# Optimization experiments

Measured on AMD Instinct MI355X. Metric: run time of the kernel, lower is better.

## Reference

```python
import jax, jax.numpy as jnp
import numpy as np

EPSILON_BASE = 0.1
N_ITERS = 10


def setup_inputs() -> dict:
    key = jax.random.key(0)
    k1, k2 = jax.random.split(key)
    N, D = 8192, 512
    embeddings = jax.random.normal(k1, (N, D), dtype=jnp.float32)
    target_noise = jax.random.normal(k2, (N, D), dtype=jnp.float32)
    return {"embeddings": embeddings, "target_noise": target_noise}


def _l2_normalize(x, axis=1, eps=1e-12):
    # matches torch.nn.functional.normalize (divide by max(norm, eps))
    norm = jnp.sqrt(jnp.sum(x * x, axis=axis, keepdims=True))
    return x / jnp.maximum(norm, eps)


def _sinkhorn(x, y):
    n, d = x.shape
    # normalize_embeddings=True path
    x = _l2_normalize(x, axis=1)
    y = _l2_normalize(y, axis=1)
    epsilon = EPSILON_BASE * 2.0
    # squared euclidean cost: C[i,j] = ||x_i - y_j||^2  (cdist p=2, squared)
    sq_x = jnp.sum(x * x, axis=1, keepdims=True)          # (n,1)
    sq_y = jnp.sum(y * y, axis=1, keepdims=True)          # (n,1)
    C = jnp.maximum(sq_x + sq_y.T - 2.0 * (x @ y.T), 0.0)  # (n,n)
    log_K = -C / epsilon

    def body(carry, _):
        log_u, log_v = carry
        log_u = -jax.nn.logsumexp(log_K + log_v[None, :], axis=1)
        log_v = -jax.nn.logsumexp(log_K.T + log_u[None, :], axis=1)
        return (log_u, log_v), None

    init = (jnp.zeros(n, dtype=x.dtype), jnp.zeros(n, dtype=y.dtype))
    (log_u, log_v), _ = jax.lax.scan(body, init, None, length=N_ITERS)

    log_P = log_u[:, None] + log_K + log_v[None, :]
    P = jnp.clip(jnp.exp(log_P), 0.0, 1.0)
    distance = jnp.sum(P * C) / n

    # nan/inf fallback: 1 - mean cosine similarity (x, y already unit norm)
    fallback = 1.0 - jnp.mean(jnp.sum(x * y, axis=1))
    bad = jnp.isnan(distance) | jnp.isinf(distance)
    return jnp.where(bad, fallback, distance)


def reference(embeddings, target_noise):
    if embeddings.ndim == 3:
        embeddings = embeddings.reshape(-1, embeddings.shape[-1])
        target_noise = target_noise.reshape(-1, target_noise.shape[-1])
    return _sinkhorn(embeddings, target_noise)
```

## Files before the change

kernel.cpp:

```cpp
#include <hip/hip_runtime.h>
#include <hip/hip_bf16.h>
#include <stdint.h>

#define NROW 8192
#define DIM  512
#define LN2   0.6931471805599453f
#define TEN_LOG2E 14.426950408889634f

typedef __attribute__((ext_vector_type(8))) short short8;
typedef __attribute__((ext_vector_type(4))) float f32x4;
typedef __attribute__((ext_vector_type(2))) float f32x2;

__global__ __launch_bounds__(256) void init_kernel(float* __restrict__ v,
                                                   float* __restrict__ diagacc,
                                                   float* __restrict__ distacc) {
  const int g = blockIdx.x * 256 + threadIdx.x;
  v[g] = 1.0f;
  if (g == 0) { diagacc[0] = 0.f; distacc[0] = 0.f; }
}

__global__ __launch_bounds__(256) void normalize_kernel(
    const float* __restrict__ X, const float* __restrict__ Y,
    __hip_bfloat16* __restrict__ Xn, __hip_bfloat16* __restrict__ Yn,
    float* __restrict__ diagacc) {
  const int wave = threadIdx.x >> 6, lane = threadIdx.x & 63;
  float dsum = 0.f;
  #pragma unroll
  for (int rr = 0; rr < 4; rr++) {
    const int row = blockIdx.x * 16 + wave * 4 + rr;
    const float4* xr = (const float4*)(X + (size_t)row * DIM);
    const float4* yr = (const float4*)(Y + (size_t)row * DIM);
    float4 x0 = xr[lane], x1 = xr[lane + 64];
    float4 y0 = yr[lane], y1 = yr[lane + 64];
    float sx = x0.x*x0.x + x0.y*x0.y + x0.z*x0.z + x0.w*x0.w
             + x1.x*x1.x + x1.y*x1.y + x1.z*x1.z + x1.w*x1.w;
    float sy = y0.x*y0.x + y0.y*y0.y + y0.z*y0.z + y0.w*y0.w
             + y1.x*y1.x + y1.y*y1.y + y1.z*y1.z + y1.w*y1.w;
    float sxy = x0.x*y0.x + x0.y*y0.y + x0.z*y0.z + x0.w*y0.w
              + x1.x*y1.x + x1.y*y1.y + x1.z*y1.z + x1.w*y1.w;
    #pragma unroll
    for (int off = 1; off < 64; off <<= 1) {
      sx  += __shfl_xor(sx, off, 64);
      sy  += __shfl_xor(sy, off, 64);
      sxy += __shfl_xor(sxy, off, 64);
    }
    const float rx = 1.0f / fmaxf(sqrtf(sx), 1e-12f);
    const float ry = 1.0f / fmaxf(sqrtf(sy), 1e-12f);
    if (lane == 0) dsum += sxy * rx * ry;
    ushort4 px, py;
    { __hip_bfloat16 b;
      b = __float2bfloat16(x0.x*rx); px.x = *(unsigned short*)&b;
      b = __float2bfloat16(x0.y*rx); px.y = *(unsigned short*)&b;
      b = __float2bfloat16(x0.z*rx); px.z = *(unsigned short*)&b;
      b = __float2bfloat16(x0.w*rx); px.w = *(unsigned short*)&b;
      b = __float2bfloat16(y0.x*ry); py.x = *(unsigned short*)&b;
      b = __float2bfloat16(y0.y*ry); py.y = *(unsigned short*)&b;
      b = __float2bfloat16(y0.z*ry); py.z = *(unsigned short*)&b;
      b = __float2bfloat16(y0.w*ry); py.w = *(unsigned short*)&b;
    }
    ((ushort4*)(Xn + (size_t)row * DIM))[lane] = px;
    ((ushort4*)(Yn + (size_t)row * DIM))[lane] = py;
    { __hip_bfloat16 b;
      b = __float2bfloat16(x1.x*rx); px.x = *(unsigned short*)&b;
      b = __float2bfloat16(x1.y*rx); px.y = *(unsigned short*)&b;
      b = __float2bfloat16(x1.z*rx); px.z = *(unsigned short*)&b;
      b = __float2bfloat16(x1.w*rx); px.w = *(unsigned short*)&b;
      b = __float2bfloat16(y1.x*ry); py.x = *(unsigned short*)&b;
      b = __float2bfloat16(y1.y*ry); py.y = *(unsigned short*)&b;
      b = __float2bfloat16(y1.z*ry); py.z = *(unsigned short*)&b;
      b = __float2bfloat16(y1.w*ry); py.w = *(unsigned short*)&b;
    }
    ((ushort4*)(Xn + (size_t)row * DIM))[lane + 64] = px;
    ((ushort4*)(Yn + (size_t)row * DIM))[lane + 64] = py;
  }
  if (lane == 0) atomicAdd(diagacc, dsum);
}

__global__ __launch_bounds__(256) void gemm_kernel(
    const __hip_bfloat16* __restrict__ A, const __hip_bfloat16* __restrict__ B,
    uint8_t* __restrict__ K) {
  __shared__ __align__(16) char smem[20480];
  short* As = (short*)smem;
  short* Bs = (short*)(smem + 10240);
  int* tileT = (int*)smem;

  const int m0 = blockIdx.y * 128;
  const int n0 = blockIdx.x * 128;
  const int t = threadIdx.x;
  const int wave = t >> 6, lane = t & 63;
  const int wm = (wave & 1) * 64, wn = (wave >> 1) * 64;
  const int fr = lane & 15;
  const int fq = lane >> 4;

  f32x4 acc[4][4];
  #pragma unroll
  for (int i = 0; i < 4; i++)
    #pragma unroll
    for (int j = 0; j < 4; j++) acc[i][j] = (f32x4)0.f;

  const int L0 = t, L1 = t + 256;
  const int ar0 = L0 >> 2, ac0 = L0 & 3;
  const int ar1 = L1 >> 2, ac1 = L1 & 3;
  const int4* Ag = (const int4*)A;
  const int4* Bg = (const int4*)B;

  for (int kt = 0; kt < 16; ++kt) {
    const int kb = kt * 4;
    int4 a0 = Ag[(size_t)(m0 + ar0) * 64 + kb + ac0];
    int4 a1 = Ag[(size_t)(m0 + ar1) * 64 + kb + ac1];
    int4 b0 = Bg[(size_t)(n0 + ar0) * 64 + kb + ac0];
    int4 b1 = Bg[(size_t)(n0 + ar1) * 64 + kb + ac1];
    __syncthreads();
    ((int4*)As)[ar0 * 5 + ac0] = a0;
    ((int4*)As)[ar1 * 5 + ac1] = a1;
    ((int4*)Bs)[ar0 * 5 + ac0] = b0;
    ((int4*)Bs)[ar1 * 5 + ac1] = b1;
    __syncthreads();
    short8 af[4], bfr[4];
    #pragma unroll
    for (int i = 0; i < 4; i++) {
      af[i]  = *(const short8*)&As[(wm + i * 16 + fr) * 40 + fq * 8];
      bfr[i] = *(const short8*)&Bs[(wn + i * 16 + fr) * 40 + fq * 8];
    }
    #pragma unroll
    for (int i = 0; i < 4; i++)
      #pragma unroll
      for (int j = 0; j < 4; j++)
        acc[i][j] = __builtin_amdgcn_mfma_f32_16x16x32_bf16(af[i], bfr[j], acc[i][j], 0, 0, 0);
  }
  __syncthreads();
  #pragma unroll
  for (int i = 0; i < 4; i++) {
    #pragma unroll
    for (int j = 0; j < 4; j++) {
      const int Rq = (wm >> 2) + i * 4 + fq;
      const int Cc = wn + j * 16 + fr;
      float v0 = exp2f(fminf(acc[i][j][0], 1.0f) * TEN_LOG2E);
      float v1 = exp2f(fminf(acc[i][j][1], 1.0f) * TEN_LOG2E);
      float v2 = exp2f(fminf(acc[i][j][2], 1.0f) * TEN_LOG2E);
      float v3 = exp2f(fminf(acc[i][j][3], 1.0f) * TEN_LOG2E);
      int pk = 0;
      pk = __builtin_amdgcn_cvt_pk_fp8_f32(v0, v1, pk, false);
      pk = __builtin_amdgcn_cvt_pk_fp8_f32(v2, v3, pk, true);
      tileT[Cc * 33 + Rq] = pk;
    }
  }
  __syncthreads();
  const int rl = t >> 1;
  const int half = t & 1;
  const int rq = rl >> 2;
  const int rb = (rl & 3) * 8;
  uint8_t* Krow = K + (size_t)(m0 + rl) * NROW + n0 + half * 64;
  #pragma unroll
  for (int q = 0; q < 4; q++) {
    int out[4];
    #pragma unroll
    for (int d = 0; d < 4; d++) {
      const int c0 = (half * 16 + q * 4 + d) * 4;
      const unsigned w0 = (unsigned)tileT[(c0 + 0) * 33 + rq];
      const unsigned w1 = (unsigned)tileT[(c0 + 1) * 33 + rq];
      const unsigned w2 = (unsigned)tileT[(c0 + 2) * 33 + rq];
      const unsigned w3 = (unsigned)tileT[(c0 + 3) * 33 + rq];
      out[d] = (int)(((w0 >> rb) & 0xffu) | (((w1 >> rb) & 0xffu) << 8)
                   | (((w2 >> rb) & 0xffu) << 16) | (((w3 >> rb) & 0xffu) << 24));
    }
    int4 o; o.x = out[0]; o.y = out[1]; o.z = out[2]; o.w = out[3];
    ((int4*)Krow)[q] = o;
  }
}

__global__ __launch_bounds__(512) void fused_pass_kernel(
    const uint8_t* __restrict__ K, const float* __restrict__ v,
    float* __restrict__ u, float* __restrict__ partials) {
  __shared__ float wsum[8][8];
  __shared__ float ubc[8];
  const int t = threadIdx.x;
  const int wave = t >> 6, lane = t & 63;
  const int i0 = blockIdx.x * 32;

  float wv[16];
  {
    const float4* vp = (const float4*)(v + t * 16);
    ((float4*)wv)[0] = vp[0]; ((float4*)wv)[1] = vp[1];
    ((float4*)wv)[2] = vp[2]; ((float4*)wv)[3] = vp[3];
  }
  float acc[16];
  #pragma unroll
  for (int c = 0; c < 16; c++) acc[c] = 0.f;

  for (int b = 0; b < 4; b++) {
    const int rbase = i0 + b * 8;
    int4 kd[8];
    #pragma unroll
    for (int r = 0; r < 8; r++)
      kd[r] = *(const int4*)(K + (size_t)(rbase + r) * NROW + t * 16);
    float dot[8];
    #pragma unroll
    for (int r = 0; r < 8; r++) {
      const int* kp = (const int*)&kd[r];
      float d0 = 0.f, d1 = 0.f;
      #pragma unroll
      for (int q = 0; q < 4; q++) {
        f32x2 lo = __builtin_amdgcn_cvt_pk_f32_fp8(kp[q], false);
        f32x2 hi = __builtin_amdgcn_cvt_pk_f32_fp8(kp[q], true);
        d0 += lo.x * wv[4 * q] + lo.y * wv[4 * q + 1];
        d1 += hi.x * wv[4 * q + 2] + hi.y * wv[4 * q + 3];
      }
      dot[r] = d0 + d1;
    }
    #pragma unroll
    for (int r = 0; r < 8; r++)
      #pragma unroll
      for (int off = 1; off < 64; off <<= 1)
        dot[r] += __shfl_xor(dot[r], off, 64);
    if (lane == 0) {
      #pragma unroll
      for (int r = 0; r < 8; r++) wsum[wave][r] = dot[r];
    }
    __syncthreads();
    if (t < 8) {
      float s = wsum[0][t] + wsum[1][t] + wsum[2][t] + wsum[3][t]
              + wsum[4][t] + wsum[5][t] + wsum[6][t] + wsum[7][t];
      float uu = 1.0f / s;
      ubc[t] = uu;
      u[rbase + t] = uu;
    }
    __syncthreads();
    float ur[8];
    #pragma unroll
    for (int r = 0; r < 8; r++) ur[r] = ubc[r];
    #pragma unroll
    for (int r = 0; r < 8; r++) {
      const int* kp = (const int*)&kd[r];
      #pragma unroll
      for (int q = 0; q < 4; q++) {
        f32x2 lo = __builtin_amdgcn_cvt_pk_f32_fp8(kp[q], false);
        f32x2 hi = __builtin_amdgcn_cvt_pk_f32_fp8(kp[q], true);
        acc[4 * q]     += lo.x * ur[r];
        acc[4 * q + 1] += lo.y * ur[r];
        acc[4 * q + 2] += hi.x * ur[r];
        acc[4 * q + 3] += hi.y * ur[r];
      }
    }
  }
  float4* pp = (float4*)(partials + (size_t)blockIdx.x * NROW + t * 16);
  pp[0] = ((float4*)acc)[0]; pp[1] = ((float4*)acc)[1];
  pp[2] = ((float4*)acc)[2]; pp[3] = ((float4*)acc)[3];
}

__global__ __launch_bounds__(256) void vreduce_kernel(
    const float* __restrict__ partials, float* __restrict__ v) {
  const int j = blockIdx.x * 256 + threadIdx.x;
  float s = 0.f;
  #pragma unroll 8
  for (int p = 0; p < 256; p++) s += partials[(size_t)p * NROW + j];
  v[j] = 1.0f / s;
}

__global__ __launch_bounds__(512) void dist_kernel(
    const uint8_t* __restrict__ K, const float* __restrict__ v,
    const float* __restrict__ u, float* __restrict__ distacc) {
  __shared__ float uld[32];
  const int t = threadIdx.x;
  const int i0 = blockIdx.x * 32;
  if (t < 32) uld[t] = u[i0 + t];
  float wv[16];
  {
    const float4* vp = (const float4*)(v + t * 16);
    ((float4*)wv)[0] = vp[0]; ((float4*)wv)[1] = vp[1];
    ((float4*)wv)[2] = vp[2]; ((float4*)wv)[3] = vp[3];
  }
  __syncthreads();
  float acc = 0.f;
  #pragma unroll 4
  for (int r = 0; r < 32; r++) {
    int4 kd = *(const int4*)(K + (size_t)(i0 + r) * NROW + t * 16);
    const float ui = uld[r];
    const int* kp = (const int*)&kd;
    #pragma unroll
    for (int q = 0; q < 4; q++) {
      f32x2 lo = __builtin_amdgcn_cvt_pk_f32_fp8(kp[q], false);
      f32x2 hi = __builtin_amdgcn_cvt_pk_f32_fp8(kp[q], true);
      float kvv[4] = {lo.x, lo.y, hi.x, hi.y};
      #pragma unroll
      for (int e = 0; e < 4; e++) {
        float kk = kvv[e];
        float p = fminf(ui * kk * wv[4 * q + e], 1.f);
        float ct = 2.f - 0.2f * LN2 * __log2f(fmaxf(kk, 1e-6f));
        acc += p * ct;
      }
    }
  }
  #pragma unroll
  for (int off = 32; off > 0; off >>= 1) acc += __shfl_down(acc, off, 64);
  __shared__ float sb[8];
  const int wave = t >> 6;
  if ((t & 63) == 0) sb[wave] = acc;
  __syncthreads();
  if (t == 0) {
    float tot = sb[0] + sb[1] + sb[2] + sb[3] + sb[4] + sb[5] + sb[6] + sb[7];
    atomicAdd(distacc, tot);
  }
}

__global__ void final_kernel(const float* __restrict__ distacc,
                             const float* __restrict__ diagacc,
                             float* __restrict__ out) {
  if (threadIdx.x == 0 && blockIdx.x == 0) {
    float d = distacc[0] * (1.0f / (float)NROW);
    float fb = 1.0f - diagacc[0] * (1.0f / (float)NROW);
    float v = (isnan(d) || isinf(d)) ? fb : d;
    __hip_bfloat16 b = __float2bfloat16(v);
    unsigned short h = *(unsigned short*)&b;
    ((unsigned int*)out)[0] = ((unsigned int)h << 16) | (unsigned int)h;
  }
}

extern "C" void kernel_launch(void* const* d_in, const int* in_sizes, int n_in,
                              void* d_out, int out_size, void* d_ws, size_t ws_size,
                              hipStream_t stream) {
  (void)in_sizes; (void)n_in; (void)out_size; (void)ws_size;
  const float* X = (const float*)d_in[0];
  const float* Y = (const float*)d_in[1];
  float* out = (float*)d_out;

  char* ws = (char*)d_ws;
  size_t off = 0;
  uint8_t* K = (uint8_t*)(ws + off);                off += (size_t)NROW * NROW;
  float* partials = (float*)(ws + off);             off += (size_t)256 * NROW * 4;
  __hip_bfloat16* Xn = (__hip_bfloat16*)(ws + off); off += (size_t)NROW * DIM * 2;
  __hip_bfloat16* Yn = (__hip_bfloat16*)(ws + off); off += (size_t)NROW * DIM * 2;
  float* uvec = (float*)(ws + off); off += NROW * 4;
  float* vvec = (float*)(ws + off); off += NROW * 4;
  float* diagacc = (float*)(ws + off); off += 256;
  float* distacc = (float*)(ws + off); off += 256;

  init_kernel<<<32, 256, 0, stream>>>(vvec, diagacc, distacc);
  normalize_kernel<<<512, 256, 0, stream>>>(X, Y, Xn, Yn, diagacc);
  gemm_kernel<<<dim3(64, 64), 256, 0, stream>>>(Xn, Yn, K);
  for (int it = 0; it < 10; ++it) {
    fused_pass_kernel<<<256, 512, 0, stream>>>(K, vvec, uvec, partials);
    vreduce_kernel<<<32, 256, 0, stream>>>(partials, vvec);
  }
  dist_kernel<<<256, 512, 0, stream>>>(K, vvec, uvec, distacc);
  final_kernel<<<1, 64, 0, stream>>>(distacc, diagacc, out);
}
```

Before: 539.1 us.

## Async LDS loads in GEMM, wider blocks and prefetch in Sinkhorn passes

The GEMM now stages A/B tiles through global_load_lds direct-to-LDS copies with a 64-wide K step, and the epilogue transpose uses a row-major tile read back with vector loads. The fused Sinkhorn pass moves to 1024-thread blocks with 8 bytes per thread and double-buffers the K row loads for the next 8-row group. The vreduce kernel splits each column's 256-partial sum across 8 thread groups in 256 blocks, and dist_kernel is widened the same way. The aim is more memory-level parallelism and lower latency, at the cost of unpadded LDS layouts that may cause bank conflicts and higher register pressure.

```diff
diff --git a/kernel.cpp b/kernel.cpp
--- a/kernel.cpp
+++ b/kernel.cpp
@@ -10,6 +10,16 @@
 typedef __attribute__((ext_vector_type(8))) short short8;
 typedef __attribute__((ext_vector_type(4))) float f32x4;
 typedef __attribute__((ext_vector_type(2))) float f32x2;
+
+__device__ __forceinline__ void barrier_lgkm() {
+  asm volatile("s_waitcnt lgkmcnt(0)\n\ts_barrier" ::: "memory");
+}
+
+__device__ __forceinline__ void async_copy16(void* lds, const void* g) {
+  __builtin_amdgcn_global_load_lds((const __attribute__((address_space(1))) void*)g,
+                                   (__attribute__((address_space(3))) void*)lds,
+                                   16, 0, 0);
+}
 
 __global__ __launch_bounds__(256) void init_kernel(float* __restrict__ v,
                                                    float* __restrict__ diagacc,
@@ -79,9 +89,9 @@
 __global__ __launch_bounds__(256) void gemm_kernel(
     const __hip_bfloat16* __restrict__ A, const __hip_bfloat16* __restrict__ B,
     uint8_t* __restrict__ K) {
-  __shared__ __align__(16) char smem[20480];
-  short* As = (short*)smem;
-  short* Bs = (short*)(smem + 10240);
+  __shared__ __align__(16) char smem[32768];
+  short* As_s = (short*)smem;
+  short* Bs_s = (short*)(smem + 16384);
   int* tileT = (int*)smem;
 
   const int m0 = blockIdx.y * 128;
@@ -98,35 +108,38 @@
     #pragma unroll
     for (int j = 0; j < 4; j++) acc[i][j] = (f32x4)0.f;
 
-  const int L0 = t, L1 = t + 256;
-  const int ar0 = L0 >> 2, ac0 = L0 & 3;
-  const int ar1 = L1 >> 2, ac1 = L1 & 3;
-  const int4* Ag = (const int4*)A;
-  const int4* Bg = (const int4*)B;
-
-  for (int kt = 0; kt < 16; ++kt) {
-    const int kb = kt * 4;
-    int4 a0 = Ag[(size_t)(m0 + ar0) * 64 + kb + ac0];
-    int4 a1 = Ag[(size_t)(m0 + ar1) * 64 + kb + ac1];
-    int4 b0 = Bg[(size_t)(n0 + ar0) * 64 + kb + ac0];
-    int4 b1 = Bg[(size_t)(n0 + ar1) * 64 + kb + ac1];
+  const char* Ab = (const char*)A;
+  const char* Bb = (const char*)B;
+  const int trow = t >> 3;
+  const int tcol = (t & 7) * 16;
+  char* AsB = (char*)As_s;
+  char* BsB = (char*)Bs_s;
+
+  for (int kt = 0; kt < 8; ++kt) {
     __syncthreads();
-    ((int4*)As)[ar0 * 5 + ac0] = a0;
-    ((int4*)As)[ar1 * 5 + ac1] = a1;
-    ((int4*)Bs)[ar0 * 5 + ac0] = b0;
-    ((int4*)Bs)[ar1 * 5 + ac1] = b1;
+    const size_t koff = (size_t)kt * 128 + tcol;
+    #pragma unroll
+    for (int c = 0; c < 4; c++) {
+      async_copy16(AsB + c * 4096 + t * 16,
+                   Ab + (size_t)(m0 + c * 32 + trow) * 1024 + koff);
+      async_copy16(BsB + c * 4096 + t * 16,
+                   Bb + (size_t)(n0 + c * 32 + trow) * 1024 + koff);
+    }
     __syncthreads();
-    short8 af[4], bfr[4];
-    #pragma unroll
-    for (int i = 0; i < 4; i++) {
-      af[i]  = *(const short8*)&As[(wm + i * 16 + fr) * 40 + fq * 8];
-      bfr[i] = *(const short8*)&Bs[(wn + i * 16 + fr) * 40 + fq * 8];
-    }
-    #pragma unroll
-    for (int i = 0; i < 4; i++)
-      #pragma unroll
-      for (int j = 0; j < 4; j++)
-        acc[i][j] = __builtin_amdgcn_mfma_f32_16x16x32_bf16(af[i], bfr[j], acc[i][j], 0, 0, 0);
+    #pragma unroll
+    for (int kk = 0; kk < 2; kk++) {
+      short8 af[4], bfr[4];
+      #pragma unroll
+      for (int i = 0; i < 4; i++) {
+        af[i]  = *(const short8*)&As_s[(wm + i * 16 + fr) * 64 + kk * 32 + fq * 8];
+        bfr[i] = *(const short8*)&Bs_s[(wn + i * 16 + fr) * 64 + kk * 32 + fq * 8];
+      }
+      #pragma unroll
+      for (int i = 0; i < 4; i++)
+        #pragma unroll
+        for (int j = 0; j < 4; j++)
+          acc[i][j] = __builtin_amdgcn_mfma_f32_16x16x32_bf16(af[i], bfr[j], acc[i][j], 0, 0, 0);
+    }
   }
   __syncthreads();
   #pragma unroll
@@ -142,7 +155,7 @@
       int pk = 0;
       pk = __builtin_amdgcn_cvt_pk_fp8_f32(v0, v1, pk, false);
       pk = __builtin_amdgcn_cvt_pk_fp8_f32(v2, v3, pk, true);
-      tileT[Cc * 33 + Rq] = pk;
+      tileT[Rq * 132 + Cc] = pk;
     }
   }
   __syncthreads();
@@ -153,60 +166,67 @@
   uint8_t* Krow = K + (size_t)(m0 + rl) * NROW + n0 + half * 64;
   #pragma unroll
   for (int q = 0; q < 4; q++) {
+    const int base = rq * 132 + half * 64 + q * 16;
+    int4 w0 = *(const int4*)&tileT[base];
+    int4 w1 = *(const int4*)&tileT[base + 4];
+    int4 w2 = *(const int4*)&tileT[base + 8];
+    int4 w3 = *(const int4*)&tileT[base + 12];
     int out[4];
+    const int* wp[4] = {(const int*)&w0, (const int*)&w1, (const int*)&w2, (const int*)&w3};
     #pragma unroll
     for (int d = 0; d < 4; d++) {
-      const int c0 = (half * 16 + q * 4 + d) * 4;
-      const unsigned w0 = (unsigned)tileT[(c0 + 0) * 33 + rq];
-      const unsigned w1 = (unsigned)tileT[(c0 + 1) * 33 + rq];
-      const unsigned w2 = (unsigned)tileT[(c0 + 2) * 33 + rq];
-      const unsigned w3 = (unsigned)tileT[(c0 + 3) * 33 + rq];
-      out[d] = (int)(((w0 >> rb) & 0xffu) | (((w1 >> rb) & 0xffu) << 8)
-                   | (((w2 >> rb) & 0xffu) << 16) | (((w3 >> rb) & 0xffu) << 24));
+      const unsigned a0 = ((unsigned)wp[d][0] >> rb) & 0xffu;
+      const unsigned a1 = ((unsigned)wp[d][1] >> rb) & 0xffu;
+      const unsigned a2 = ((unsigned)wp[d][2] >> rb) & 0xffu;
+      const unsigned a3 = ((unsigned)wp[d][3] >> rb) & 0xffu;
+      out[d] = (int)(a0 | (a1 << 8) | (a2 << 16) | (a3 << 24));
     }
     int4 o; o.x = out[0]; o.y = out[1]; o.z = out[2]; o.w = out[3];
     ((int4*)Krow)[q] = o;
   }
 }
 
-__global__ __launch_bounds__(512) void fused_pass_kernel(
+__global__ __launch_bounds__(1024) void fused_pass_kernel(
     const uint8_t* __restrict__ K, const float* __restrict__ v,
     float* __restrict__ u, float* __restrict__ partials) {
-  __shared__ float wsum[8][8];
+  __shared__ float wsum[16][8];
   __shared__ float ubc[8];
   const int t = threadIdx.x;
   const int wave = t >> 6, lane = t & 63;
   const int i0 = blockIdx.x * 32;
 
-  float wv[16];
+  float wv[8];
   {
-    const float4* vp = (const float4*)(v + t * 16);
+    const float4* vp = (const float4*)(v + t * 8);
     ((float4*)wv)[0] = vp[0]; ((float4*)wv)[1] = vp[1];
-    ((float4*)wv)[2] = vp[2]; ((float4*)wv)[3] = vp[3];
-  }
-  float acc[16];
-  #pragma unroll
-  for (int c = 0; c < 16; c++) acc[c] = 0.f;
-
+  }
+  float acc[8];
+  #pragma unroll
+  for (int c = 0; c < 8; c++) acc[c] = 0.f;
+
+  int2 kd[2][8];
+  #pragma unroll
+  for (int r = 0; r < 8; r++)
+    kd[0][r] = *(const int2*)(K + (size_t)(i0 + r) * NROW + t * 8);
+
+  #pragma unroll
   for (int b = 0; b < 4; b++) {
-    const int rbase = i0 + b * 8;
-    int4 kd[8];
-    #pragma unroll
-    for (int r = 0; r < 8; r++)
-      kd[r] = *(const int4*)(K + (size_t)(rbase + r) * NROW + t * 16);
+    const int cb = b & 1, nb = cb ^ 1;
+    if (b < 3) {
+      #pragma unroll
+      for (int r = 0; r < 8; r++)
+        kd[nb][r] = *(const int2*)(K + (size_t)(i0 + (b + 1) * 8 + r) * NROW + t * 8);
+    }
     float dot[8];
     #pragma unroll
     for (int r = 0; r < 8; r++) {
-      const int* kp = (const int*)&kd[r];
-      float d0 = 0.f, d1 = 0.f;
-      #pragma unroll
-      for (int q = 0; q < 4; q++) {
-        f32x2 lo = __builtin_amdgcn_cvt_pk_f32_fp8(kp[q], false);
-        f32x2 hi = __builtin_amdgcn_cvt_pk_f32_fp8(kp[q], true);
-        d0 += lo.x * wv[4 * q] + lo.y * wv[4 * q + 1];
-        d1 += hi.x * wv[4 * q + 2] + hi.y * wv[4 * q + 3];
-      }
-      dot[r] = d0 + d1;
+      const int* kp = (const int*)&kd[cb][r];
+      f32x2 l0 = __builtin_amdgcn_cvt_pk_f32_fp8(kp[0], false);
+      f32x2 h0 = __builtin_amdgcn_cvt_pk_f32_fp8(kp[0], true);
+      f32x2 l1 = __builtin_amdgcn_cvt_pk_f32_fp8(kp[1], false);
+      f32x2 h1 = __builtin_amdgcn_cvt_pk_f32_fp8(kp[1], true);
+      dot[r] = l0.x * wv[0] + l0.y * wv[1] + h0.x * wv[2] + h0.y * wv[3]
+             + l1.x * wv[4] + l1.y * wv[5] + h1.x * wv[6] + h1.y * wv[7];
     }
     #pragma unroll
     for (int r = 0; r < 8; r++)
@@ -217,88 +237,96 @@
       #pragma unroll
       for (int r = 0; r < 8; r++) wsum[wave][r] = dot[r];
     }
-    __syncthreads();
+    barrier_lgkm();
     if (t < 8) {
-      float s = wsum[0][t] + wsum[1][t] + wsum[2][t] + wsum[3][t]
-              + wsum[4][t] + wsum[5][t] + wsum[6][t] + wsum[7][t];
+      float s = 0.f;
+      #pragma unroll
+      for (int w = 0; w < 16; w++) s += wsum[w][t];
       float uu = 1.0f / s;
       ubc[t] = uu;
-      u[rbase + t] = uu;
-    }
-    __syncthreads();
-    float ur[8];
-    #pragma unroll
-    for (int r = 0; r < 8; r++) ur[r] = ubc[r];
+      u[i0 + b * 8 + t] = uu;
+    }
+    barrier_lgkm();
     #pragma unroll
     for (int r = 0; r < 8; r++) {
-      const int* kp = (const int*)&kd[r];
-      #pragma unroll
-      for (int q = 0; q < 4; q++) {
-        f32x2 lo = __builtin_amdgcn_cvt_pk_f32_fp8(kp[q], false);
-        f32x2 hi = __builtin_amdgcn_cvt_pk_f32_fp8(kp[q], true);
-        acc[4 * q]     += lo.x * ur[r];
-        acc[4 * q + 1] += lo.y * ur[r];
-        acc[4 * q + 2] += hi.x * ur[r];
-        acc[4 * q + 3] += hi.y * ur[r];
-      }
-    }
-  }
-  float4* pp = (float4*)(partials + (size_t)blockIdx.x * NROW + t * 16);
-  pp[0] = ((float4*)acc)[0]; pp[1] = ((float4*)acc)[1];
-  pp[2] = ((float4*)acc)[2]; pp[3] = ((float4*)acc)[3];
+      const float ur = ubc[r];
+      const int* kp = (const int*)&kd[cb][r];
+      f32x2 l0 = __builtin_amdgcn_cvt_pk_f32_fp8(kp[0], false);
+      f32x2 h0 = __builtin_amdgcn_cvt_pk_f32_fp8(kp[0], true);
+      f32x2 l1 = __builtin_amdgcn_cvt_pk_f32_fp8(kp[1], false);
+      f32x2 h1 = __builtin_amdgcn_cvt_pk_f32_fp8(kp[1], true);
+      acc[0] += l0.x * ur; acc[1] += l0.y * ur;
+      acc[2] += h0.x * ur; acc[3] += h0.y * ur;
+      acc[4] += l1.x * ur; acc[5] += l1.y * ur;
+      acc[6] += h1.x * ur; acc[7] += h1.y * ur;
+    }
+  }
+  float4* pp = (float4*)(partials + (size_t)blockIdx.x * NROW + t * 8);
+  pp[0] = ((float4*)acc)[0];
+  pp[1] = ((float4*)acc)[1];
 }
 
 __global__ __launch_bounds__(256) void vreduce_kernel(
     const float* __restrict__ partials, float* __restrict__ v) {
-  const int j = blockIdx.x * 256 + threadIdx.x;
+  __shared__ float red[8][32];
+  const int t = threadIdx.x;
+  const int c = t & 31, g = t >> 5;
+  const int j = blockIdx.x * 32 + c;
   float s = 0.f;
   #pragma unroll 8
-  for (int p = 0; p < 256; p++) s += partials[(size_t)p * NROW + j];
-  v[j] = 1.0f / s;
-}
-
-__global__ __launch_bounds__(512) void dist_kernel(
+  for (int p = g * 32; p < g * 32 + 32; p++) s += partials[(size_t)p * NROW + j];
+  red[g][c] = s;
+  __syncthreads();
+  if (t < 32) {
+    float tot = 0.f;
+    #pragma unroll
+    for (int gg = 0; gg < 8; gg++) tot += red[gg][t];
+    v[blockIdx.x * 32 + t] = 1.0f / tot;
+  }
+}
+
+__global__ __launch_bounds__(1024) void dist_kernel(
     const uint8_t* __restrict__ K, const float* __restrict__ v,
     const float* __restrict__ u, float* __restrict__ distacc) {
   __shared__ float uld[32];
   const int t = threadIdx.x;
   const int i0 = blockIdx.x * 32;
   if (t < 32) uld[t] = u[i0 + t];
-  float wv[16];
+  float wv[8];
   {
-    const float4* vp = (const float4*)(v + t * 16);
+    const float4* vp = (const float4*)(v + t * 8);
     ((float4*)wv)[0] = vp[0]; ((float4*)wv)[1] = vp[1];
-    ((float4*)wv)[2] = vp[2]; ((float4*)wv)[3] = vp[3];
   }
   __syncthreads();
   float acc = 0.f;
   #pragma unroll 4
   for (int r = 0; r < 32; r++) {
-    int4 kd = *(const int4*)(K + (size_t)(i0 + r) * NROW + t * 16);
+    int2 kdv = *(const int2*)(K + (size_t)(i0 + r) * NROW + t * 8);
     const float ui = uld[r];
-    const int* kp = (const int*)&kd;
-    #pragma unroll
-    for (int q = 0; q < 4; q++) {
-      f32x2 lo = __builtin_amdgcn_cvt_pk_f32_fp8(kp[q], false);
-      f32x2 hi = __builtin_amdgcn_cvt_pk_f32_fp8(kp[q], true);
-      float kvv[4] = {lo.x, lo.y, hi.x, hi.y};
-      #pragma unroll
-      for (int e = 0; e < 4; e++) {
-        float kk = kvv[e];
-        float p = fminf(ui * kk * wv[4 * q + e], 1.f);
-        float ct = 2.f - 0.2f * LN2 * __log2f(fmaxf(kk, 1e-6f));
-        acc += p * ct;
-      }
+    const int* kp = (const int*)&kdv;
+    f32x2 l0 = __builtin_amdgcn_cvt_pk_f32_fp8(kp[0], false);
+    f32x2 h0 = __builtin_amdgcn_cvt_pk_f32_fp8(kp[0], true);
+    f32x2 l1 = __builtin_amdgcn_cvt_pk_f32_fp8(kp[1], false);
+    f32x2 h1 = __builtin_amdgcn_cvt_pk_f32_fp8(kp[1], true);
+    float kvv[8] = {l0.x, l0.y, h0.x, h0.y, l1.x, l1.y, h1.x, h1.y};
+    #pragma unroll
+    for (int e = 0; e < 8; e++) {
+      float kk = kvv[e];
+      float p = fminf(ui * kk * wv[e], 1.f);
+      float ct = 2.f - 0.2f * LN2 * __log2f(fmaxf(kk, 1e-6f));
+      acc += p * ct;
     }
   }
   #pragma unroll
   for (int off = 32; off > 0; off >>= 1) acc += __shfl_down(acc, off, 64);
-  __shared__ float sb[8];
+  __shared__ float sb[16];
   const int wave = t >> 6;
   if ((t & 63) == 0) sb[wave] = acc;
   __syncthreads();
   if (t == 0) {
-    float tot = sb[0] + sb[1] + sb[2] + sb[3] + sb[4] + sb[5] + sb[6] + sb[7];
+    float tot = 0.f;
+    #pragma unroll
+    for (int w = 0; w < 16; w++) tot += sb[w];
     atomicAdd(distacc, tot);
   }
 }
@@ -339,9 +367,9 @@
   normalize_kernel<<<512, 256, 0, stream>>>(X, Y, Xn, Yn, diagacc);
   gemm_kernel<<<dim3(64, 64), 256, 0, stream>>>(Xn, Yn, K);
   for (int it = 0; it < 10; ++it) {
-    fused_pass_kernel<<<256, 512, 0, stream>>>(K, vvec, uvec, partials);
-    vreduce_kernel<<<32, 256, 0, stream>>>(partials, vvec);
-  }
-  dist_kernel<<<256, 512, 0, stream>>>(K, vvec, uvec, distacc);
+    fused_pass_kernel<<<256, 1024, 0, stream>>>(K, vvec, uvec, partials);
+    vreduce_kernel<<<256, 256, 0, stream>>>(partials, vvec);
+  }
+  dist_kernel<<<256, 1024, 0, stream>>>(K, vvec, uvec, distacc);
   final_kernel<<<1, 64, 0, stream>>>(distacc, diagacc, out);
 }
```

Measured after the change: 1.442 ms. 167% more time.
